# Kernel tuning notes

Hardware: AMD Instinct MI355X
Metric: run time of the kernel (lower is better)

The kernel has to match this reference:

```python
import jax, jax.numpy as jnp
import numpy as np

NEG_SLOPE = 0.01  # F.leaky_relu default
DROP_P = 0.5      # F.dropout(p=0.5, training=True by default in this code)


def _lrelu(x):
    return jnp.where(x >= 0, x, NEG_SLOPE * x)


def _hconv(Xi, X, Ht, Hs, edge_w, theta, w_trans, bias):
    # Faithful to Ht.T @ diag(edge_w) @ Hs @ X @ theta + Xi @ w_trans + bias,
    # with diag(edge_w) fused as a per-row scale of the [E, out] intermediate.
    msg = (Hs @ X) @ theta                 # [E, out]
    agg = Ht.T @ (edge_w[:, None] * msg)   # [N, out]
    return _lrelu(agg + Xi @ w_trans + bias)


def setup_inputs() -> dict:
    key = jax.random.key(0)
    ks = jax.random.split(key, 14)
    N, E, F0, H = 8192, 4096, 128, 128
    f32 = jnp.float32
    return {
        "xi": jax.random.normal(ks[0], (N, F0), f32),
        "x": jax.random.normal(ks[1], (N, F0), f32),
        "Ht": jax.random.uniform(ks[2], (E, N), f32),
        "Hs": jax.random.uniform(ks[3], (E, N), f32),
        "state": jax.random.normal(ks[4], (N, 1), f32),
        # conv0 params (std=0.01 init as in torch code)
        "w_trans0": 0.01 * jax.random.normal(ks[5], (F0, H), f32),
        "theta0": 0.01 * jax.random.normal(ks[6], (F0, H), f32),
        "edge_w0": jnp.ones((E,), f32),
        "bias0": 0.01 * jax.random.normal(ks[7], (H,), f32),
        # conv1 params
        "w_trans1": 0.01 * jax.random.normal(ks[8], (H, H), f32),
        "theta1": 0.01 * jax.random.normal(ks[9], (H, H), f32),
        "edge_w1": jnp.ones((E,), f32),
        "bias1": 0.01 * jax.random.normal(ks[10], (H,), f32),
        # fc: Linear(H+1, 1)
        "fc_w": 0.01 * jax.random.normal(ks[11], (H + 1, 1), f32),
        "fc_b": 0.01 * jax.random.normal(ks[12], (1,), f32),
    }


def reference(xi, x, Ht, Hs, state,
              w_trans0, theta0, edge_w0, bias0,
              w_trans1, theta1, edge_w1, bias1,
              fc_w, fc_b):
    X1 = _hconv(xi, x, Ht, Hs, edge_w0, theta0, w_trans0, bias0)  # [N, H]
    # F.dropout(p=0.5) is active (training=True default); fixed mask for determinism
    keep = jax.random.bernoulli(jax.random.key(42), 1.0 - DROP_P, X1.shape)
    X1 = jnp.where(keep, X1 / (1.0 - DROP_P), 0.0)
    X2 = _hconv(xi, X1, Ht, Hs, edge_w1, theta1, w_trans1, bias1)  # [N, H]
    X = _lrelu(X2)  # second leaky_relu, as in DQN.forward
    Xc = jnp.concatenate([X, state], axis=1)  # [N, H+1]
    return Xc @ fc_w + fc_b  # [N, 1]
```

## Files before the change

kernel.cpp:

```cpp
#include <hip/hip_runtime.h>
#include <stdint.h>


typedef short short8 __attribute__((ext_vector_type(8)));
typedef float f32x4 __attribute__((ext_vector_type(4)));

static constexpr int N = 8192, E = 4096, F = 128;
static constexpr int SA = 16, SB = 8;

__device__ __forceinline__ unsigned rotl32(unsigned x, int r) {
  return (x << r) | (x >> (32 - r));
}

__device__ __forceinline__ uint2 threefry2x32(unsigned k0, unsigned k1,
                                              unsigned x0, unsigned x1) {
  unsigned ks[3] = {k0, k1, k0 ^ k1 ^ 0x1BD11BDAu};
  x0 += ks[0];
  x1 += ks[1];
  const int R0[4] = {13, 15, 26, 6};
  const int R1[4] = {17, 29, 16, 24};
#pragma unroll
  for (int i = 0; i < 5; ++i) {
#pragma unroll
    for (int j = 0; j < 4; ++j) {
      const int r = (i % 2 == 0) ? R0[j] : R1[j];
      x0 += x1;
      x1 = rotl32(x1, r);
      x1 ^= x0;
    }
    x0 += ks[(i + 1) % 3];
    x1 += ks[(i + 2) % 3] + (unsigned)(i + 1);
  }
  return make_uint2(x0, x1);
}

__device__ __forceinline__ float drop_scale(unsigned idx) {
  const uint2 o = threefry2x32(0u, 42u, 0u, idx);
  return ((o.x ^ o.y) & 0x80000000u) ? 0.0f : 2.0f;
}

__device__ __forceinline__ float lrelu(float v) {
  return v >= 0.0f ? v : 0.01f * v;
}

__device__ __forceinline__ unsigned rne1(float a) {
  unsigned ua = __builtin_bit_cast(unsigned, a);
  ua += 0x7fffu + ((ua >> 16) & 1u);
  return ua >> 16;
}
__device__ __forceinline__ float bf16_val(unsigned u16) {
  return __builtin_bit_cast(float, u16 << 16);
}
__device__ __forceinline__ unsigned pk_bf16(float a, float b) {
  return rne1(a) | (rne1(b) << 16);
}
__device__ __forceinline__ void split2(float a, float b, unsigned& hi,
                                       unsigned& lo) {
  const unsigned ha = rne1(a), hb = rne1(b);
  const float ra = a - bf16_val(ha), rb = b - bf16_val(hb);
  hi = ha | (hb << 16);
  lo = rne1(ra) | (rne1(rb) << 16);
}

template <bool TRANSA>
__global__ __launch_bounds__(512, 4) void big_gemm(
    const float* __restrict__ A, const float* __restrict__ Bt,
    float* __restrict__ P, int M, int K, int lda, int kchunk) {
  __shared__ __align__(16) short As[2][128 * 40];
  __shared__ __align__(16) short Bh[2][128 * 40];
  __shared__ __align__(16) short Bl[2][128 * 40];

  const int tid = threadIdx.x;
  const int lane = tid & 63;
  const int w = tid >> 6;
  const int wm = (w & 3) << 5;
  const int wn = (w >> 2) << 6;
  const int l15 = lane & 15;
  const int koff = (lane >> 4) << 3;

  const int r0 = blockIdx.x * 128;
  const int s = blockIdx.y;
  const int kbeg = s * kchunk;
  const int nt = kchunk >> 5;

  float4 ra[2], rb[2];

  auto loadg = [&](int kt) {
    if (!TRANSA) {
#pragma unroll
      for (int i = 0; i < 2; ++i) {
        const int f = i * 512 + tid;
        const int m = f >> 3;
        const int kq = f & 7;
        ra[i] = *(const float4*)(A + (size_t)(r0 + m) * lda + kt + 4 * kq);
      }
    } else {
      const int m = tid & 127;
      const int eo = tid >> 7;
      float* v = (float*)ra;
#pragma unroll
      for (int r = 0; r < 8; ++r)
        v[r] = A[(size_t)(kt + 8 * eo + r) * lda + r0 + m];
    }
#pragma unroll
    for (int i = 0; i < 2; ++i) {
      const int q = i * 512 + tid;
      const int c = q >> 3;
      const int kq = q & 7;
      rb[i] = *(const float4*)(Bt + (size_t)c * K + kt + 4 * kq);
    }
  };

  auto store_lds = [&](int buf) {
    if (!TRANSA) {
#pragma unroll
      for (int i = 0; i < 2; ++i) {
        const int f = i * 512 + tid;
        const int m = f >> 3;
        const int kq = f & 7;
        uint2 u = {pk_bf16(ra[i].x, ra[i].y), pk_bf16(ra[i].z, ra[i].w)};
        *(uint2*)&As[buf][m * 40 + 4 * kq] = u;
      }
    } else {
      const int m = tid & 127;
      const int eo = tid >> 7;
      const float* v = (const float*)ra;
      uint4 u = {pk_bf16(v[0], v[1]), pk_bf16(v[2], v[3]),
                 pk_bf16(v[4], v[5]), pk_bf16(v[6], v[7])};
      *(uint4*)&As[buf][m * 40 + 8 * eo] = u;
    }
#pragma unroll
    for (int i = 0; i < 2; ++i) {
      const int q = i * 512 + tid;
      const int c = q >> 3;
      const int kq = q & 7;
      uint2 uh, ul;
      split2(rb[i].x, rb[i].y, uh.x, ul.x);
      split2(rb[i].z, rb[i].w, uh.y, ul.y);
      *(uint2*)&Bh[buf][c * 40 + 4 * kq] = uh;
      *(uint2*)&Bl[buf][c * 40 + 4 * kq] = ul;
    }
  };

  f32x4 acc[2][4];
#pragma unroll
  for (int i = 0; i < 2; ++i)
#pragma unroll
    for (int j = 0; j < 4; ++j) acc[i][j] = (f32x4){0.f, 0.f, 0.f, 0.f};

  loadg(kbeg);
  store_lds(0);
  int cur = 0;
  for (int t = 0; t < nt; ++t) {
    __syncthreads();
    if (t + 1 < nt) loadg(kbeg + 32 * (t + 1));

    short8 af[2], bhf[4], blf[4];
#pragma unroll
    for (int i = 0; i < 2; ++i)
      af[i] = *(const short8*)&As[cur][(wm + 16 * i + l15) * 40 + koff];
#pragma unroll
    for (int j = 0; j < 4; ++j) {
      bhf[j] = *(const short8*)&Bh[cur][(wn + 16 * j + l15) * 40 + koff];
      blf[j] = *(const short8*)&Bl[cur][(wn + 16 * j + l15) * 40 + koff];
    }
#pragma unroll
    for (int i = 0; i < 2; ++i)
#pragma unroll
      for (int j = 0; j < 4; ++j) {
        acc[i][j] = __builtin_amdgcn_mfma_f32_16x16x32_bf16(af[i], blf[j],
                                                            acc[i][j], 0, 0, 0);
        acc[i][j] = __builtin_amdgcn_mfma_f32_16x16x32_bf16(af[i], bhf[j],
                                                            acc[i][j], 0, 0, 0);
      }
    if (t + 1 < nt) store_lds(cur ^ 1);
    cur ^= 1;
  }

  const int rquad = (lane >> 4) << 2;
#pragma unroll
  for (int i = 0; i < 2; ++i)
#pragma unroll
    for (int j = 0; j < 4; ++j)
#pragma unroll
      for (int r = 0; r < 4; ++r) {
        const int row = r0 + wm + 16 * i + rquad + r;
        const int col = wn + 16 * j + l15;
        P[((size_t)s * M + row) * 128 + col] = acc[i][j][r];
      }
}

template <bool WA>
__device__ __forceinline__ void small_core(
    const float* __restrict__ src, const float* __restrict__ W,
    const float* __restrict__ bias, float* __restrict__ out, short* WTh,
    short* WTl, short* Xh, short* Xl, int n0, int tid) {
  constexpr int TI = WA ? 4 : 2;
  constexpr int TJ = WA ? 2 : 4;
  const int lane = tid & 63;
  const int w = tid >> 6;
  const int l15 = lane & 15;
  const int wm = (w & 1) * (WA ? 64 : 32);
  const int wn = (w >> 1) * (WA ? 32 : 64);

  f32x4 acc[TI][TJ];
#pragma unroll
  for (int i = 0; i < TI; ++i)
#pragma unroll
    for (int j = 0; j < TJ; ++j) acc[i][j] = (f32x4){0.f, 0.f, 0.f, 0.f};

  for (int k0 = 0; k0 < 128; k0 += 32) {
#pragma unroll
    for (int i = 0; i < 2; ++i) {
      const int f = i * 256 + tid;
      const int c = f & 127;
      const int eo = f >> 7;
      uint4 uh, ul;
      unsigned* ph = (unsigned*)&uh;
      unsigned* pl = (unsigned*)&ul;
#pragma unroll
      for (int r = 0; r < 4; ++r) {
        const float a = W[(size_t)(k0 + 8 * eo + 2 * r) * 128 + c];
        const float b = W[(size_t)(k0 + 8 * eo + 2 * r + 1) * 128 + c];
        split2(a, b, ph[r], pl[r]);
      }
      *(uint4*)&WTh[c * 40 + 8 * eo] = uh;
      *(uint4*)&WTl[c * 40 + 8 * eo] = ul;
    }
#pragma unroll
    for (int i = 0; i < 2; ++i) {
      const int q = i * 256 + tid;
      const int n = q >> 3;
      const int kq = q & 7;
      const float4 v =
          *(const float4*)(src + (size_t)(n0 + n) * 128 + k0 + 4 * kq);
      uint2 uh, ul;
      split2(v.x, v.y, uh.x, ul.x);
      split2(v.z, v.w, uh.y, ul.y);
      *(uint2*)&Xh[n * 40 + 4 * kq] = uh;
      *(uint2*)&Xl[n * 40 + 4 * kq] = ul;
    }
    __syncthreads();

    const int koff = (lane >> 4) << 3;
    short8 ah[TI], al[TI], bh[TJ], bl[TJ];
#pragma unroll
    for (int i = 0; i < TI; ++i) {
      const int m = wm + 16 * i + l15;
      ah[i] = WA ? *(const short8*)&WTh[m * 40 + koff]
                 : *(const short8*)&Xh[m * 40 + koff];
      al[i] = WA ? *(const short8*)&WTl[m * 40 + koff]
                 : *(const short8*)&Xl[m * 40 + koff];
    }
#pragma unroll
    for (int j = 0; j < TJ; ++j) {
      const int c = wn + 16 * j + l15;
      bh[j] = WA ? *(const short8*)&Xh[c * 40 + koff]
                 : *(const short8*)&WTh[c * 40 + koff];
      bl[j] = WA ? *(const short8*)&Xl[c * 40 + koff]
                 : *(const short8*)&WTl[c * 40 + koff];
    }
#pragma unroll
    for (int i = 0; i < TI; ++i)
#pragma unroll
      for (int j = 0; j < TJ; ++j) {
        acc[i][j] = __builtin_amdgcn_mfma_f32_16x16x32_bf16(al[i], bh[j],
                                                            acc[i][j], 0, 0, 0);
        acc[i][j] = __builtin_amdgcn_mfma_f32_16x16x32_bf16(ah[i], bl[j],
                                                            acc[i][j], 0, 0, 0);
        acc[i][j] = __builtin_amdgcn_mfma_f32_16x16x32_bf16(ah[i], bh[j],
                                                            acc[i][j], 0, 0, 0);
      }
    __syncthreads();
  }

  const int rquad = (lane >> 4) << 2;
#pragma unroll
  for (int i = 0; i < TI; ++i)
#pragma unroll
    for (int j = 0; j < TJ; ++j)
#pragma unroll
      for (int r = 0; r < 4; ++r) {
        const int row = wm + 16 * i + rquad + r;
        const int col = wn + 16 * j + l15;
        if constexpr (WA)
          out[(size_t)row * N + n0 + col] = acc[i][j][r];
        else
          out[(size_t)(n0 + row) * 128 + col] = acc[i][j][r] + bias[col];
      }
}

__global__ __launch_bounds__(256) void small_fused(
    const float* __restrict__ srcT, const float* __restrict__ Wth,
    const float* __restrict__ srcB, const float* __restrict__ Wwt,
    const float* __restrict__ bias, float* __restrict__ Tt,
    float* __restrict__ Badd) {
  __shared__ __align__(16) short WTh[128 * 40], WTl[128 * 40];
  __shared__ __align__(16) short Xh[64 * 40], Xl[64 * 40];
  const int n0 = blockIdx.x * 64;
  if (blockIdx.y == 0)
    small_core<true>(srcT, Wth, nullptr, Tt, WTh, WTl, Xh, Xl, n0,
                     threadIdx.x);
  else
    small_core<false>(srcB, Wwt, bias, Badd, WTh, WTl, Xh, Xl, n0,
                      threadIdx.x);
}

__global__ __launch_bounds__(256) void reduce_A(const float* __restrict__ P,
                                                const float* __restrict__ ew,
                                                float* __restrict__ Mt) {
  __shared__ float Lt[16 * 132];
  const int tid = threadIdx.x;
  const int e0 = blockIdx.x * 16;
#pragma unroll
  for (int i = 0; i < 2; ++i) {
    const int f = i * 256 + tid;
    const int el = f >> 5;
    const int cq = f & 31;
    float4 a = {0.f, 0.f, 0.f, 0.f};
#pragma unroll
    for (int s = 0; s < SA; ++s) {
      const float4 v =
          *(const float4*)(P + ((size_t)s * E + e0 + el) * 128 + 4 * cq);
      a.x += v.x; a.y += v.y; a.z += v.z; a.w += v.w;
    }
    const float sc = ew[e0 + el];
    a.x *= sc; a.y *= sc; a.z *= sc; a.w *= sc;
    *(float4*)&Lt[el * 132 + 4 * cq] = a;
  }
  __syncthreads();
#pragma unroll
  for (int i = 0; i < 2; ++i) {
    const int g = i * 256 + tid;
    const int c = g >> 2;
    const int eq = g & 3;
    float4 o;
    o.x = Lt[(4 * eq + 0) * 132 + c];
    o.y = Lt[(4 * eq + 1) * 132 + c];
    o.z = Lt[(4 * eq + 2) * 132 + c];
    o.w = Lt[(4 * eq + 3) * 132 + c];
    *(float4*)&Mt[(size_t)c * E + e0 + 4 * eq] = o;
  }
}

__global__ __launch_bounds__(256) void reduce_B1(const float* __restrict__ P,
                                                 const float* __restrict__ Badd,
                                                 float* __restrict__ X1) {
  const int q = blockIdx.x * 256 + threadIdx.x;
  const int n = q >> 5;
  const int cq = q & 31;
  float4 a = {0.f, 0.f, 0.f, 0.f};
#pragma unroll
  for (int s = 0; s < SB; ++s) {
    const float4 v = *(const float4*)(P + ((size_t)s * N + n) * 128 + 4 * cq);
    a.x += v.x; a.y += v.y; a.z += v.z; a.w += v.w;
  }
  const float4 b = *(const float4*)(Badd + (size_t)n * 128 + 4 * cq);
  const unsigned fb = (unsigned)(n * 128 + 4 * cq);
  float4 o;
  o.x = lrelu(a.x + b.x) * drop_scale(fb + 0u);
  o.y = lrelu(a.y + b.y) * drop_scale(fb + 1u);
  o.z = lrelu(a.z + b.z) * drop_scale(fb + 2u);
  o.w = lrelu(a.w + b.w) * drop_scale(fb + 3u);
  *(float4*)&X1[(size_t)n * 128 + 4 * cq] = o;
}

__global__ __launch_bounds__(256) void reduce_B2(
    const float* __restrict__ P, const float* __restrict__ Badd,
    const float* __restrict__ fcw, const float* __restrict__ state,
    const float* __restrict__ fcb, float* __restrict__ out) {
  __shared__ float part[4];
  const int tid = threadIdx.x;
  const int nn = tid >> 7;
  const int c = tid & 127;
  const int n = blockIdx.x * 2 + nn;
  float v = 0.f;
#pragma unroll
  for (int s = 0; s < SB; ++s) v += P[((size_t)s * N + n) * 128 + c];
  v += Badd[(size_t)n * 128 + c];
  float p = lrelu(lrelu(v)) * fcw[c];
#pragma unroll
  for (int m = 32; m >= 1; m >>= 1) p += __shfl_xor(p, m, 64);
  if ((tid & 63) == 0) part[tid >> 6] = p;
  __syncthreads();
  if (tid < 2)
    out[blockIdx.x * 2 + tid] = part[2 * tid] + part[2 * tid + 1] +
                                state[blockIdx.x * 2 + tid] * fcw[128] + fcb[0];
}

extern "C" void kernel_launch(void* const* d_in, const int* in_sizes, int n_in,
                              void* d_out, int out_size, void* d_ws,
                              size_t ws_size, hipStream_t stream) {
  (void)in_sizes; (void)n_in; (void)out_size; (void)ws_size;

  const float* xi = (const float*)d_in[0];
  const float* x = (const float*)d_in[1];
  const float* Ht = (const float*)d_in[2];
  const float* Hs = (const float*)d_in[3];
  const float* state = (const float*)d_in[4];
  const float* wt0 = (const float*)d_in[5];
  const float* th0 = (const float*)d_in[6];
  const float* ew0 = (const float*)d_in[7];
  const float* bi0 = (const float*)d_in[8];
  const float* wt1 = (const float*)d_in[9];
  const float* th1 = (const float*)d_in[10];
  const float* ew1 = (const float*)d_in[11];
  const float* bi1 = (const float*)d_in[12];
  const float* fcw = (const float*)d_in[13];
  const float* fcb = (const float*)d_in[14];
  float* out = (float*)d_out;

  float* ws = (float*)d_ws;
  float* P = ws;
  float* Tt = P + (size_t)SA * E * F;
  float* Badd = Tt + (size_t)F * N;
  float* Mt = Badd + (size_t)N * F;
  float* X1 = Mt + (size_t)F * E;

  small_fused<<<dim3(N / 64, 2), 256, 0, stream>>>(x, th0, xi, wt0, bi0, Tt,
                                                   Badd);
  big_gemm<false><<<dim3(E / 128, SA), 512, 0, stream>>>(Hs, Tt, P, E, N, N,
                                                         N / SA);
  reduce_A<<<E / 16, 256, 0, stream>>>(P, ew0, Mt);
  big_gemm<true><<<dim3(N / 128, SB), 512, 0, stream>>>(Ht, Mt, P, N, E, N,
                                                        E / SB);
  reduce_B1<<<N * F / 4 / 256, 256, 0, stream>>>(P, Badd, X1);

  small_fused<<<dim3(N / 64, 2), 256, 0, stream>>>(X1, th1, xi, wt1, bi1, Tt,
                                                   Badd);
  big_gemm<false><<<dim3(E / 128, SA), 512, 0, stream>>>(Hs, Tt, P, E, N, N,
                                                         N / SA);
  reduce_A<<<E / 16, 256, 0, stream>>>(P, ew1, Mt);
  big_gemm<true><<<dim3(N / 128, SB), 512, 0, stream>>>(Ht, Mt, P, N, E, N,
                                                        E / SB);
  reduce_B2<<<N / 2, 256, 0, stream>>>(P, Badd, fcw, state, fcb, out);
}
```

Baseline: 448.0 us.

## Pre-split B operands to bf16 tiles and triple-buffer big GEMM with direct-to-LDS loads

```diff
diff --git a/kernel.cpp b/kernel.cpp
--- a/kernel.cpp
+++ b/kernel.cpp
@@ -7,6 +7,15 @@
 
 static constexpr int N = 8192, E = 4096, F = 128;
 static constexpr int SA = 16, SB = 8;
+
+#define ASM_VMCNT(n) asm volatile("s_waitcnt vmcnt(" #n ")" ::: "memory")
+#define ASM_LGKM0() asm volatile("s_waitcnt lgkmcnt(0)" ::: "memory")
+
+__device__ __forceinline__ void gload_lds16(const short* g, short* l) {
+  __builtin_amdgcn_global_load_lds(
+      (const __attribute__((address_space(1))) unsigned int*)g,
+      (__attribute__((address_space(3))) unsigned int*)l, 16, 0, 0);
+}
 
 __device__ __forceinline__ unsigned rotl32(unsigned x, int r) {
   return (x << r) | (x >> (32 - r));
@@ -61,14 +70,18 @@
   hi = ha | (hb << 16);
   lo = rne1(ra) | (rne1(rb) << 16);
 }
+__device__ __forceinline__ void split1(float a, unsigned& h, unsigned& l) {
+  h = rne1(a);
+  l = rne1(a - bf16_val(h));
+}
 
 template <bool TRANSA>
 __global__ __launch_bounds__(512, 4) void big_gemm(
-    const float* __restrict__ A, const float* __restrict__ Bt,
-    float* __restrict__ P, int M, int K, int lda, int kchunk) {
-  __shared__ __align__(16) short As[2][128 * 40];
-  __shared__ __align__(16) short Bh[2][128 * 40];
-  __shared__ __align__(16) short Bl[2][128 * 40];
+    const float* __restrict__ A, const short* __restrict__ Bhg,
+    const short* __restrict__ Blg, float* __restrict__ P, int M, int lda) {
+  __shared__ __align__(16) short As[3][4096];
+  __shared__ __align__(16) short Bhs[3][4096];
+  __shared__ __align__(16) short Bls[3][4096];
 
   const int tid = threadIdx.x;
   const int lane = tid & 63;
@@ -76,108 +89,116 @@
   const int wm = (w & 3) << 5;
   const int wn = (w >> 2) << 6;
   const int l15 = lane & 15;
-  const int koff = (lane >> 4) << 3;
-
+  const int q = lane >> 4;
   const int r0 = blockIdx.x * 128;
+  constexpr int NT = 16;
+  const int kt0 = blockIdx.y * NT;
+
+  const int m0a = tid >> 3;
+  const int m0b = (512 + tid) >> 3;
+  const int kq0 = tid & 7;
+  const int m1 = tid & 127;
+  const int eo1 = tid >> 7;
+
+  float Rf[2][8];
+
+  auto loadA = [&](float* R, int kt) {
+    if constexpr (!TRANSA) {
+      *(float4*)&R[0] =
+          *(const float4*)(A + (size_t)(r0 + m0a) * lda + kt * 32 + 4 * kq0);
+      *(float4*)&R[4] =
+          *(const float4*)(A + (size_t)(r0 + m0b) * lda + kt * 32 + 4 * kq0);
+    } else {
+#pragma unroll
+      for (int r = 0; r < 8; ++r)
+        R[r] = A[(size_t)(kt * 32 + 8 * eo1 + r) * lda + r0 + m1];
+    }
+  };
+  auto packA = [&](const float* R, int buf) {
+    if constexpr (!TRANSA) {
+      const int s0 = (kq0 >> 1) ^ ((m0a >> 1) & 3);
+      uint2 u0 = {pk_bf16(R[0], R[1]), pk_bf16(R[2], R[3])};
+      *(uint2*)&As[buf][m0a * 32 + s0 * 8 + (kq0 & 1) * 4] = u0;
+      const int s1 = (kq0 >> 1) ^ ((m0b >> 1) & 3);
+      uint2 u1 = {pk_bf16(R[4], R[5]), pk_bf16(R[6], R[7])};
+      *(uint2*)&As[buf][m0b * 32 + s1 * 8 + (kq0 & 1) * 4] = u1;
+    } else {
+      const int s0 = eo1 ^ ((m1 >> 1) & 3);
+      uint4 u = {pk_bf16(R[0], R[1]), pk_bf16(R[2], R[3]),
+                 pk_bf16(R[4], R[5]), pk_bf16(R[6], R[7])};
+      *(uint4*)&As[buf][m1 * 32 + s0 * 8] = u;
+    }
+  };
+  auto stageB = [&](int buf, int kt) {
+    const size_t g = (size_t)kt * 4096 + w * 512 + lane * 8;
+    gload_lds16(Bhg + g, &Bhs[buf][w * 512]);
+    gload_lds16(Blg + g, &Bls[buf][w * 512]);
+  };
+
+  f32x4 acc[2][4];
+#pragma unroll
+  for (int i = 0; i < 2; ++i)
+#pragma unroll
+    for (int j = 0; j < 4; ++j) acc[i][j] = (f32x4){0.f, 0.f, 0.f, 0.f};
+
+  loadA(Rf[0], kt0 + 0);
+  stageB(0, kt0 + 0);
+  loadA(Rf[1], kt0 + 1);
+  stageB(1, kt0 + 1);
+  if constexpr (!TRANSA) ASM_VMCNT(4); else ASM_VMCNT(10);
+  __builtin_amdgcn_sched_barrier(0);
+  packA(Rf[0], 0);
+  ASM_LGKM0();
+  __builtin_amdgcn_s_barrier();
+
+  auto step = [&](int i, float* Ri, float* Rp) {
+    const int cur = i % 3, nxt = (i + 1) % 3, nn = (i + 2) % 3;
+    if (i + 2 < NT) {
+      loadA(Ri, kt0 + i + 2);
+      stageB(nn, kt0 + i + 2);
+    }
+    __builtin_amdgcn_sched_barrier(0);
+    short8 af[2], bh[4], bl[4];
+#pragma unroll
+    for (int ii = 0; ii < 2; ++ii) {
+      const int m = wm + 16 * ii + l15;
+      af[ii] = *(const short8*)&As[cur][m * 32 + ((q ^ ((m >> 1) & 3)) << 3)];
+    }
+#pragma unroll
+    for (int j = 0; j < 4; ++j) {
+      const int c = wn + 16 * j + l15;
+      bh[j] = *(const short8*)&Bhs[cur][c * 32 + (q << 3)];
+      bl[j] = *(const short8*)&Bls[cur][c * 32 + (q << 3)];
+    }
+#pragma unroll
+    for (int ii = 0; ii < 2; ++ii)
+#pragma unroll
+      for (int j = 0; j < 4; ++j) {
+        acc[ii][j] = __builtin_amdgcn_mfma_f32_16x16x32_bf16(af[ii], bl[j],
+                                                             acc[ii][j], 0, 0, 0);
+        acc[ii][j] = __builtin_amdgcn_mfma_f32_16x16x32_bf16(af[ii], bh[j],
+                                                             acc[ii][j], 0, 0, 0);
+      }
+    if (i + 1 < NT) {
+      if (i + 2 < NT) {
+        if constexpr (!TRANSA) ASM_VMCNT(4); else ASM_VMCNT(10);
+      } else {
+        ASM_VMCNT(0);
+      }
+      __builtin_amdgcn_sched_barrier(0);
+      packA(Rp, nxt);
+    }
+    ASM_LGKM0();
+    __builtin_amdgcn_s_barrier();
+  };
+
+  for (int ib = 0; ib < NT; ib += 2) {
+    step(ib, Rf[0], Rf[1]);
+    step(ib + 1, Rf[1], Rf[0]);
+  }
+
   const int s = blockIdx.y;
-  const int kbeg = s * kchunk;
-  const int nt = kchunk >> 5;
-
-  float4 ra[2], rb[2];
-
-  auto loadg = [&](int kt) {
-    if (!TRANSA) {
-#pragma unroll
-      for (int i = 0; i < 2; ++i) {
-        const int f = i * 512 + tid;
-        const int m = f >> 3;
-        const int kq = f & 7;
-        ra[i] = *(const float4*)(A + (size_t)(r0 + m) * lda + kt + 4 * kq);
-      }
-    } else {
-      const int m = tid & 127;
-      const int eo = tid >> 7;
-      float* v = (float*)ra;
-#pragma unroll
-      for (int r = 0; r < 8; ++r)
-        v[r] = A[(size_t)(kt + 8 * eo + r) * lda + r0 + m];
-    }
-#pragma unroll
-    for (int i = 0; i < 2; ++i) {
-      const int q = i * 512 + tid;
-      const int c = q >> 3;
-      const int kq = q & 7;
-      rb[i] = *(const float4*)(Bt + (size_t)c * K + kt + 4 * kq);
-    }
-  };
-
-  auto store_lds = [&](int buf) {
-    if (!TRANSA) {
-#pragma unroll
-      for (int i = 0; i < 2; ++i) {
-        const int f = i * 512 + tid;
-        const int m = f >> 3;
-        const int kq = f & 7;
-        uint2 u = {pk_bf16(ra[i].x, ra[i].y), pk_bf16(ra[i].z, ra[i].w)};
-        *(uint2*)&As[buf][m * 40 + 4 * kq] = u;
-      }
-    } else {
-      const int m = tid & 127;
-      const int eo = tid >> 7;
-      const float* v = (const float*)ra;
-      uint4 u = {pk_bf16(v[0], v[1]), pk_bf16(v[2], v[3]),
-                 pk_bf16(v[4], v[5]), pk_bf16(v[6], v[7])};
-      *(uint4*)&As[buf][m * 40 + 8 * eo] = u;
-    }
-#pragma unroll
-    for (int i = 0; i < 2; ++i) {
-      const int q = i * 512 + tid;
-      const int c = q >> 3;
-      const int kq = q & 7;
-      uint2 uh, ul;
-      split2(rb[i].x, rb[i].y, uh.x, ul.x);
-      split2(rb[i].z, rb[i].w, uh.y, ul.y);
-      *(uint2*)&Bh[buf][c * 40 + 4 * kq] = uh;
-      *(uint2*)&Bl[buf][c * 40 + 4 * kq] = ul;
-    }
-  };
-
-  f32x4 acc[2][4];
-#pragma unroll
-  for (int i = 0; i < 2; ++i)
-#pragma unroll
-    for (int j = 0; j < 4; ++j) acc[i][j] = (f32x4){0.f, 0.f, 0.f, 0.f};
-
-  loadg(kbeg);
-  store_lds(0);
-  int cur = 0;
-  for (int t = 0; t < nt; ++t) {
-    __syncthreads();
-    if (t + 1 < nt) loadg(kbeg + 32 * (t + 1));
-
-    short8 af[2], bhf[4], blf[4];
-#pragma unroll
-    for (int i = 0; i < 2; ++i)
-      af[i] = *(const short8*)&As[cur][(wm + 16 * i + l15) * 40 + koff];
-#pragma unroll
-    for (int j = 0; j < 4; ++j) {
-      bhf[j] = *(const short8*)&Bh[cur][(wn + 16 * j + l15) * 40 + koff];
-      blf[j] = *(const short8*)&Bl[cur][(wn + 16 * j + l15) * 40 + koff];
-    }
-#pragma unroll
-    for (int i = 0; i < 2; ++i)
-#pragma unroll
-      for (int j = 0; j < 4; ++j) {
-        acc[i][j] = __builtin_amdgcn_mfma_f32_16x16x32_bf16(af[i], blf[j],
-                                                            acc[i][j], 0, 0, 0);
-        acc[i][j] = __builtin_amdgcn_mfma_f32_16x16x32_bf16(af[i], bhf[j],
-                                                            acc[i][j], 0, 0, 0);
-      }
-    if (t + 1 < nt) store_lds(cur ^ 1);
-    cur ^= 1;
-  }
-
-  const int rquad = (lane >> 4) << 2;
+  const int rquad = q << 2;
 #pragma unroll
   for (int i = 0; i < 2; ++i)
 #pragma unroll
@@ -193,8 +214,9 @@
 template <bool WA>
 __device__ __forceinline__ void small_core(
     const float* __restrict__ src, const float* __restrict__ W,
-    const float* __restrict__ bias, float* __restrict__ out, short* WTh,
-    short* WTl, short* Xh, short* Xl, int n0, int tid) {
+    const float* __restrict__ bias, float* __restrict__ out,
+    short* __restrict__ outH, short* __restrict__ outL, short* WTh, short* WTl,
+    short* Xh, short* Xl, int n0, int tid) {
   constexpr int TI = WA ? 4 : 2;
   constexpr int TJ = WA ? 2 : 4;
   const int lane = tid & 63;
@@ -229,9 +251,9 @@
     }
 #pragma unroll
     for (int i = 0; i < 2; ++i) {
-      const int q = i * 256 + tid;
-      const int n = q >> 3;
-      const int kq = q & 7;
+      const int qq = i * 256 + tid;
+      const int n = qq >> 3;
+      const int kq = qq & 7;
       const float4 v =
           *(const float4*)(src + (size_t)(n0 + n) * 128 + k0 + 4 * kq);
       uint2 uh, ul;
@@ -278,45 +300,55 @@
 #pragma unroll
   for (int i = 0; i < TI; ++i)
 #pragma unroll
-    for (int j = 0; j < TJ; ++j)
-#pragma unroll
-      for (int r = 0; r < 4; ++r) {
-        const int row = wm + 16 * i + rquad + r;
-        const int col = wn + 16 * j + l15;
-        if constexpr (WA)
-          out[(size_t)row * N + n0 + col] = acc[i][j][r];
-        else
+    for (int j = 0; j < TJ; ++j) {
+      if constexpr (WA) {
+        const int colg = n0 + wn + 16 * j + l15;
+        const size_t tb = (size_t)(colg >> 5) * 4096 + (colg & 31);
+#pragma unroll
+        for (int r = 0; r < 4; ++r) {
+          const int row = wm + 16 * i + rquad + r;
+          unsigned h, l;
+          split1(acc[i][j][r], h, l);
+          outH[tb + (size_t)row * 32] = (short)h;
+          outL[tb + (size_t)row * 32] = (short)l;
+        }
+      } else {
+#pragma unroll
+        for (int r = 0; r < 4; ++r) {
+          const int row = wm + 16 * i + rquad + r;
+          const int col = wn + 16 * j + l15;
           out[(size_t)(n0 + row) * 128 + col] = acc[i][j][r] + bias[col];
-      }
+        }
+      }
+    }
 }
 
 __global__ __launch_bounds__(256) void small_fused(
     const float* __restrict__ srcT, const float* __restrict__ Wth,
     const float* __restrict__ srcB, const float* __restrict__ Wwt,
-    const float* __restrict__ bias, float* __restrict__ Tt,
-    float* __restrict__ Badd) {
+    const float* __restrict__ bias, short* __restrict__ TtH,
+    short* __restrict__ TtL, float* __restrict__ Badd) {
   __shared__ __align__(16) short WTh[128 * 40], WTl[128 * 40];
   __shared__ __align__(16) short Xh[64 * 40], Xl[64 * 40];
   const int n0 = blockIdx.x * 64;
   if (blockIdx.y == 0)
-    small_core<true>(srcT, Wth, nullptr, Tt, WTh, WTl, Xh, Xl, n0,
-                     threadIdx.x);
+    small_core<true>(srcT, Wth, nullptr, nullptr, TtH, TtL, WTh, WTl, Xh, Xl,
+                     n0, threadIdx.x);
   else
-    small_core<false>(srcB, Wwt, bias, Badd, WTh, WTl, Xh, Xl, n0,
-                      threadIdx.x);
+    small_core<false>(srcB, Wwt, bias, Badd, nullptr, nullptr, WTh, WTl, Xh, Xl,
+                      n0, threadIdx.x);
 }
 
 __global__ __launch_bounds__(256) void reduce_A(const float* __restrict__ P,
                                                 const float* __restrict__ ew,
-                                                float* __restrict__ Mt) {
-  __shared__ float Lt[16 * 132];
+                                                short* __restrict__ MtH,
+                                                short* __restrict__ MtL) {
+  __shared__ float Lt[8 * 132];
   const int tid = threadIdx.x;
-  const int e0 = blockIdx.x * 16;
-#pragma unroll
-  for (int i = 0; i < 2; ++i) {
-    const int f = i * 256 + tid;
-    const int el = f >> 5;
-    const int cq = f & 31;
+  const int e0 = blockIdx.x * 8;
+  {
+    const int el = tid >> 5;
+    const int cq = tid & 31;
     float4 a = {0.f, 0.f, 0.f, 0.f};
 #pragma unroll
     for (int s = 0; s < SA; ++s) {
@@ -329,17 +361,21 @@
     *(float4*)&Lt[el * 132 + 4 * cq] = a;
   }
   __syncthreads();
-#pragma unroll
-  for (int i = 0; i < 2; ++i) {
-    const int g = i * 256 + tid;
-    const int c = g >> 2;
-    const int eq = g & 3;
+  {
+    const int c = tid >> 1;
+    const int eq = tid & 1;
+    const int eb = e0 + 4 * eq;
     float4 o;
     o.x = Lt[(4 * eq + 0) * 132 + c];
     o.y = Lt[(4 * eq + 1) * 132 + c];
     o.z = Lt[(4 * eq + 2) * 132 + c];
     o.w = Lt[(4 * eq + 3) * 132 + c];
-    *(float4*)&Mt[(size_t)c * E + e0 + 4 * eq] = o;
+    uint2 uh, ul;
+    split2(o.x, o.y, uh.x, ul.x);
+    split2(o.z, o.w, uh.y, ul.y);
+    const size_t off = (size_t)(eb >> 5) * 4096 + (size_t)c * 32 + (eb & 31);
+    *(uint2*)&MtH[off] = uh;
+    *(uint2*)&MtL[off] = ul;
   }
 }
 
@@ -412,26 +448,24 @@
 
   float* ws = (float*)d_ws;
   float* P = ws;
-  float* Tt = P + (size_t)SA * E * F;
-  float* Badd = Tt + (size_t)F * N;
-  float* Mt = Badd + (size_t)N * F;
-  float* X1 = Mt + (size_t)F * E;
-
-  small_fused<<<dim3(N / 64, 2), 256, 0, stream>>>(x, th0, xi, wt0, bi0, Tt,
-                                                   Badd);
-  big_gemm<false><<<dim3(E / 128, SA), 512, 0, stream>>>(Hs, Tt, P, E, N, N,
-                                                         N / SA);
-  reduce_A<<<E / 16, 256, 0, stream>>>(P, ew0, Mt);
-  big_gemm<true><<<dim3(N / 128, SB), 512, 0, stream>>>(Ht, Mt, P, N, E, N,
-                                                        E / SB);
+  short* TtH = (short*)(P + (size_t)8388608);
+  short* TtL = TtH + (size_t)1048576;
+  short* MtH = TtL + (size_t)1048576;
+  short* MtL = MtH + (size_t)524288;
+  float* Badd = (float*)(MtL + (size_t)524288);
+  float* X1 = Badd + (size_t)N * 128;
+
+  small_fused<<<dim3(N / 64, 2), 256, 0, stream>>>(x, th0, xi, wt0, bi0, TtH,
+                                                   TtL, Badd);
+  big_gemm<false><<<dim3(E / 128, SA), 512, 0, stream>>>(Hs, TtH, TtL, P, E, N);
+  reduce_A<<<E / 8, 256, 0, stream>>>(P, ew0, MtH, MtL);
+  big_gemm<true><<<dim3(N / 128, SB), 512, 0, stream>>>(Ht, MtH, MtL, P, N, N);
   reduce_B1<<<N * F / 4 / 256, 256, 0, stream>>>(P, Badd, X1);
 
-  small_fused<<<dim3(N / 64, 2), 256, 0, stream>>>(X1, th1, xi, wt1, bi1, Tt,
-                                                   Badd);
-  big_gemm<false><<<dim3(E / 128, SA), 512, 0, stream>>>(Hs, Tt, P, E, N, N,
-                                                         N / SA);
-  reduce_A<<<E / 16, 256, 0, stream>>>(P, ew1, Mt);
-  big_gemm<true><<<dim3(N / 128, SB), 512, 0, stream>>>(Ht, Mt, P, N, E, N,
-                                                        E / SB);
+  small_fused<<<dim3(N / 64, 2), 256, 0, stream>>>(X1, th1, xi, wt1, bi1, TtH,
+                                                   TtL, Badd);
+  big_gemm<false><<<dim3(E / 128, SA), 512, 0, stream>>>(Hs, TtH, TtL, P, E, N);
+  reduce_A<<<E / 8, 256, 0, stream>>>(P, ew1, MtH, MtL);
+  big_gemm<true><<<dim3(N / 128, SB), 512, 0, stream>>>(Ht, MtH, MtL, P, N, N);
   reduce_B2<<<N / 2, 256, 0, stream>>>(P, Badd, fcw, state, fcb, out);
 }
```

After: 458.2 us. +2.3%, slower.
